# Optimization experiments

Hardware: AMD Instinct MI355X
Metric: run time of the kernel (lower is better)

## Reference

```python
import jax, jax.numpy as jnp
import numpy as np

# Dims: N batch, I input channels, C = in/hidden/attention/projection/out channels (all 128),
# streams=1, groups=1, spatial kernel 3, dropout 0.
N, I, C, H, W = 8, 128, 128, 36, 36


def _conv(x, w, pad):
    # x: [N, Cin, H, W], w: [Cout, Cin, kh, kw]
    return jax.lax.conv_general_dilated(
        x, w, (1, 1), pad, dimension_numbers=("NCHW", "OIHW", "NCHW"))


def _bias(b):
    return b[None, :, None, None]


def setup_inputs() -> dict:
    key = jax.random.key(0)
    ks = jax.random.split(key, 16)
    std = 0.05

    def w(k, o, i, s):
        return jax.random.normal(k, (o, i, s, s), jnp.float32) * std

    p = {}
    p["inp"] = jax.random.normal(ks[0], (N, I, H, W), jnp.float32)
    p["c0"] = jax.random.normal(ks[1], (1, C, 1, 1), jnp.float32)
    # proj_x: 1x1 conv input->in_channels, bias init 0
    p["w_x"] = w(ks[2], C, I, 1)
    p["b_x"] = jnp.zeros((C,), jnp.float32)
    # token convs (3x3, no bias); q uses SAME pad, k/v VALID
    p["w_qx"] = w(ks[3], C, C, 3)
    p["w_qc"] = w(ks[4], C, C, 3)
    scale = C ** (-0.5)  # gain = attn_channels^-0.5 on k projections
    p["w_kx"] = w(ks[5], C, C, 3) * scale
    p["w_kc"] = w(ks[6], C, C, 3) * scale
    p["w_vx"] = w(ks[7], C, C, 3)
    p["w_vc"] = w(ks[8], C, C, 3)
    # gating 1x1 convs: proj_z (bias=init_gate=1), proj_n (bias=0), in 2*proj channels
    p["w_z"] = w(ks[9], C, 2 * C, 1)
    p["b_z"] = jnp.ones((C,), jnp.float32)
    p["w_n"] = w(ks[10], C, 2 * C, 1)
    p["b_n"] = jnp.zeros((C,), jnp.float32)
    # proj_h: in_channels + 2*projection_channels -> hidden
    p["w_h"] = w(ks[11], C, 3 * C, 1)
    p["b_h"] = jnp.zeros((C,), jnp.float32)
    # output 1x1 conv hidden -> out_channels
    p["w_o"] = w(ks[12], C, C, 1)
    p["b_o"] = jnp.zeros((C,), jnp.float32)
    return p


def reference(inp, c0, w_x, b_x, w_qx, w_qc, w_kx, w_kc, w_vx, w_vc,
              w_z, b_z, w_n, b_n, w_h, b_h, w_o, b_o):
    # proj_x (1x1) -> x: [N, C, H, W]
    x = _conv(inp, w_x, "VALID") + _bias(b_x)
    n_, _, hh, ww = x.shape
    c = jnp.broadcast_to(c0, (n_, c0.shape[1], hh, ww))
    q_len = hh * ww
    # q: SAME pad -> Q = H*W tokens; k/v: VALID -> D = (H-2)*(W-2) tokens
    q = jnp.stack([_conv(x, w_qx, "SAME"), _conv(c, w_qc, "SAME")], 0)
    q = q.reshape(2, n_, -1, q_len)                      # [A, N, C, Q]
    k_x = _conv(x, w_kx, "VALID")
    d_len = k_x.shape[2] * k_x.shape[3]
    k = jnp.stack([k_x, _conv(c, w_kc, "VALID")], 0).reshape(2, n_, -1, d_len)   # [B, N, C, D]
    v = jnp.stack([_conv(x, w_vx, "VALID"), _conv(c, w_vc, "VALID")], 0)
    v = v.reshape(2, n_, -1, d_len)                      # [B, N, C, D]
    # all (A query source) x (B key/value source) attention pairs
    attn = jax.nn.softmax(jnp.einsum("ancq,bncd->anbqd", q, k), axis=-1)
    a = jnp.einsum("bncd,anbqd->anbcq", v, attn)         # [A, N, B, C, Q]
    a = a.reshape(2, n_, -1, hh, ww)                     # channels = B*C = 2*proj
    a_x, a_c = a[0], a[1]
    # GRU-style gated cell update (stored state; not part of the returned output)
    z = jax.nn.sigmoid(_conv(a_c, w_z, "VALID") + _bias(b_z))
    n_cand = jnp.tanh(_conv(a_c, w_n, "VALID") + _bias(b_n))
    c_new = z * c + (1.0 - z) * n_cand  # noqa: F841 (past['c'] in the original)
    # hidden: tanh(proj_h(cat[x, a_x])), dropout p=0 is identity
    xa = jnp.concatenate([x, a_x], axis=1)               # [N, 3*C, H, W]
    h = jnp.tanh(_conv(xa, w_h, "VALID") + _bias(b_h))
    return _conv(h, w_o, "VALID") + _bias(b_o)           # [N, C, H, W]
```

## Files before the change

### kernel.cpp

```cpp
#include <hip/hip_runtime.h>
#include <hip/hip_bf16.h>
#include <math.h>

#define NN 8
#define CH 128
#define HH 36
#define WWI 36
#define PP 1296
#define DD 1156
#define VP 1280
#define KC 1152
#define QT 81
#define DT 5

typedef __attribute__((ext_vector_type(8))) short short8;
typedef __attribute__((ext_vector_type(4))) float f32x4;

__device__ inline unsigned short f2bf(float f) {
    __hip_bfloat16 h = __float2bfloat16(f);
    return __builtin_bit_cast(unsigned short, h);
}
__device__ inline float fast_tanh(float x) {
    float e = __expf(2.f * x);
    return 1.f - 2.f / (e + 1.f);
}
#define MFMA(a, b, c) __builtin_amdgcn_mfma_f32_16x16x32_bf16((a), (b), (c), 0, 0, 0)

__global__ void k_setup(const float* __restrict__ wq, const float* __restrict__ wk,
                        const float* __restrict__ wv, const float* __restrict__ wh,
                        const float* __restrict__ wo, const float* __restrict__ wx,
                        const float* __restrict__ c0, const float* __restrict__ w_vc,
                        const float* __restrict__ b_h,
                        unsigned short* __restrict__ wcat, unsigned short* __restrict__ whb,
                        unsigned short* __restrict__ wob, unsigned short* __restrict__ wxb,
                        float* __restrict__ hconst)
{
    if (blockIdx.x == 576) {
        __shared__ float c0s[CH];
        __shared__ float part[256];
        __shared__ float vcs[CH];
        const int t = threadIdx.x;
        const int c = t & 127, half = t >> 7;
        if (t < CH) c0s[t] = c0[t];
        __syncthreads();
        {
            const float* row = w_vc + (size_t)c * 1152 + half * 576;
            float s = 0.f;
#pragma unroll 4
            for (int j4 = 0; j4 < 144; ++j4) {
                float4 v = ((const float4*)row)[j4];
                int j = half * 576 + j4 * 4;
                s += v.x * c0s[j / 9] + v.y * c0s[(j + 1) / 9]
                   + v.z * c0s[(j + 2) / 9] + v.w * c0s[(j + 3) / 9];
            }
            part[t] = s;
        }
        __syncthreads();
        if (t < CH) vcs[t] = part[t] + part[t + 128];
        __syncthreads();
        {
            const float* wrow = wh + (size_t)c * 384 + 256 + half * 64;
            float hs = 0.f;
#pragma unroll
            for (int j4 = 0; j4 < 16; ++j4) {
                float4 v = ((const float4*)wrow)[j4];
                int ci = half * 64 + j4 * 4;
                hs += v.x * vcs[ci] + v.y * vcs[ci + 1] + v.z * vcs[ci + 2] + v.w * vcs[ci + 3];
            }
            part[t] = hs;
        }
        __syncthreads();
        if (t < CH) hconst[t] = b_h[t] + part[t] + part[t + 128];
        return;
    }
    int t = blockIdx.x * 256 + threadIdx.x;
    int co = t / KC;
    int rem = t - co * KC;
    int tap = rem >> 7, ci = rem & 127;
    int iidx = co * KC + ci * 9 + tap;
    wcat[t] = f2bf(wq[iidx]);
    wcat[147456 + t] = f2bf(wk[iidx]);
    wcat[294912 + t] = f2bf(wv[iidx]);
    if (t < 32768) {
        int c2 = t >> 8, k2 = t & 255;
        whb[t] = f2bf(wh[c2 * 384 + k2]);
    }
    if (t < 16384) { wob[t] = f2bf(wo[t]); wxb[t] = f2bf(wx[t]); }
}

__global__ __launch_bounds__(64)
void k_proj(const float* __restrict__ inp, const unsigned short* __restrict__ wxb,
            const float* __restrict__ bx, unsigned short* __restrict__ xt)
{
    const int lane = threadIdx.x;
    const int quad = lane >> 4, lrow = lane & 15;
    const int p0 = blockIdx.x * 16;
    const int co0 = blockIdx.y * 64;
    const int n = blockIdx.z;
    const float* in_n = inp + (size_t)n * CH * PP;
    f32x4 acc[4] = {};

#pragma unroll
    for (int ks = 0; ks < 4; ++ks) {
        union { short8 v; unsigned short u[8]; } a;
        int ci0 = ks * 32 + quad * 8;
#pragma unroll
        for (int j = 0; j < 8; ++j)
            a.u[j] = f2bf(in_n[(size_t)(ci0 + j) * PP + p0 + lrow]);
#pragma unroll
        for (int ni = 0; ni < 4; ++ni) {
            short8 b = *(const short8*)&wxb[(size_t)(co0 + ni * 16 + lrow) * CH + ks * 32 + quad * 8];
            acc[ni] = MFMA(a.v, b, acc[ni]);
        }
    }
    unsigned short* xn = xt + (size_t)n * PP * CH;
#pragma unroll
    for (int ni = 0; ni < 4; ++ni) {
        float bv = bx[co0 + ni * 16 + lrow];
#pragma unroll
        for (int r = 0; r < 4; ++r)
            xn[(size_t)(p0 + quad * 4 + r) * CH + co0 + ni * 16 + lrow] = f2bf(acc[ni][r] + bv);
    }
}

__global__ __launch_bounds__(256)
void k_conv(const unsigned short* __restrict__ xt, const unsigned short* __restrict__ wcat,
            unsigned short* __restrict__ qt, unsigned short* __restrict__ kt,
            unsigned short* __restrict__ vb)
{
    __shared__ unsigned short lA[2][64 * 72];
    const int t = threadIdx.x;
    const int wave = t >> 6, lane = t & 63;
    const int quad = lane >> 4, lrow = lane & 15;
    const int mode = blockIdx.y;
    const int n = blockIdx.z;
    const int limit = (mode == 0) ? PP : DD;
    const int tile0 = blockIdx.x * 64;
    if (tile0 >= limit) return;
    const unsigned short* xn = xt + (size_t)n * PP * CH;
    const unsigned short* wb = wcat + (size_t)mode * 128 * KC;

    const int arow = t >> 2, aseg = t & 3;
    int apr, apc;
    {
        int tok = tile0 + arow; if (tok >= limit) tok = limit - 1;
        int dv = (mode == 0) ? 36 : 34;
        apr = tok / dv; apc = tok - apr * dv;
    }
    const unsigned short* wr0 = wb + (size_t)((wave * 2 + 0) * 16 + lrow) * KC;
    const unsigned short* wr1 = wb + (size_t)((wave * 2 + 1) * 16 + lrow) * KC;

    uint4 ra0, ra1;
    auto loadA = [&](int ks) {
        int tap = ks >> 1;
        int ky = tap / 3, kx = tap - ky * 3;
        int ci = (ks & 1) * 64 + aseg * 16;
        if (mode == 0) {
            int yy = apr + ky - 1, xx = apc + kx - 1;
            bool ok = (yy >= 0) && (yy < HH) && (xx >= 0) && (xx < WWI);
            ra0 = make_uint4(0, 0, 0, 0);
            ra1 = make_uint4(0, 0, 0, 0);
            if (ok) {
                const unsigned short* p = &xn[(size_t)(yy * WWI + xx) * CH + ci];
                ra0 = *(const uint4*)p;
                ra1 = *(const uint4*)(p + 8);
            }
        } else {
            int yy = apr + ky, xx = apc + kx;
            const unsigned short* p = &xn[(size_t)(yy * WWI + xx) * CH + ci];
            ra0 = *(const uint4*)p;
            ra1 = *(const uint4*)(p + 8);
        }
    };
    auto storeA = [&](int buf) {
        *(uint4*)&lA[buf][arow * 72 + aseg * 16] = ra0;
        *(uint4*)&lA[buf][arow * 72 + aseg * 16 + 8] = ra1;
    };

    short8 b0[2], b1[2], n0[2], n1[2];
    auto loadB = [&](int ks, short8* d0, short8* d1) {
        int off = (ks >> 1) * 128 + (ks & 1) * 64 + quad * 8;
        d0[0] = *(const short8*)(wr0 + off);
        d0[1] = *(const short8*)(wr0 + off + 32);
        d1[0] = *(const short8*)(wr1 + off);
        d1[1] = *(const short8*)(wr1 + off + 32);
    };

    f32x4 acc[4][2] = {};
    loadA(0);
    storeA(0);
    loadB(0, b0, b1);
    __syncthreads();

#pragma unroll
    for (int ks = 0; ks < 18; ++ks) {
        const int buf = ks & 1;
        if (ks < 17) {
            loadA(ks + 1);
            loadB(ks + 1, n0, n1);
        }
#pragma unroll
        for (int sub = 0; sub < 2; ++sub)
#pragma unroll
            for (int mi = 0; mi < 4; ++mi) {
                short8 a = *(const short8*)&lA[buf][(mi * 16 + lrow) * 72 + sub * 32 + quad * 8];
                acc[mi][0] = MFMA(a, b0[sub], acc[mi][0]);
                acc[mi][1] = MFMA(a, b1[sub], acc[mi][1]);
            }
        if (ks < 17) {
            storeA(buf ^ 1);
            b0[0] = n0[0]; b0[1] = n0[1];
            b1[0] = n1[0]; b1[1] = n1[1];
        }
        __syncthreads();
    }

    if (mode == 0) {
        unsigned short* qn = qt + (size_t)n * PP * CH;
#pragma unroll
        for (int mi = 0; mi < 4; ++mi)
#pragma unroll
            for (int r = 0; r < 4; ++r) {
                int p = tile0 + mi * 16 + quad * 4 + r;
                if (p < PP)
#pragma unroll
                    for (int ni = 0; ni < 2; ++ni)
                        qn[(size_t)p * CH + (wave * 2 + ni) * 16 + lrow] = f2bf(acc[mi][ni][r]);
            }
    } else if (mode == 1) {
        unsigned short* kn = kt + (size_t)n * DD * CH;
#pragma unroll
        for (int mi = 0; mi < 4; ++mi)
#pragma unroll
            for (int r = 0; r < 4; ++r) {
                int d = tile0 + mi * 16 + quad * 4 + r;
                if (d < DD)
#pragma unroll
                    for (int ni = 0; ni < 2; ++ni)
                        kn[(size_t)d * CH + (wave * 2 + ni) * 16 + lrow] = f2bf(acc[mi][ni][r]);
            }
    } else {
        unsigned short* vn = vb + (size_t)n * CH * VP;
#pragma unroll
        for (int mi = 0; mi < 4; ++mi)
#pragma unroll
            for (int r = 0; r < 4; ++r) {
                int d = tile0 + mi * 16 + quad * 4 + r;
                if (d < DD)
#pragma unroll
                    for (int ni = 0; ni < 2; ++ni)
                        vn[(size_t)((wave * 2 + ni) * 16 + lrow) * VP + d] = f2bf(acc[mi][ni][r]);
            }
    }
}

__global__ __launch_bounds__(256)
void k_attn(const unsigned short* __restrict__ qt, const unsigned short* __restrict__ kt,
            const unsigned short* __restrict__ vb, _Float16* __restrict__ po,
            float* __restrict__ pm, float* __restrict__ pl)
{
    __shared__ unsigned short lS[2][128 * 40];
    __shared__ unsigned short lp[4][16 * 136];
    const int t = threadIdx.x;
    const int wave = t >> 6, lane = t & 63;
    const int quad = lane >> 4, lrow = lane & 15;
    const int qg = blockIdx.x;
    const int dt = blockIdx.y;
    const int n = blockIdx.z;
    const int qti = qg * 4 + wave;
    const int d0 = dt * 256;
    const unsigned short* qn = qt + (size_t)n * PP * CH;
    const unsigned short* kn = kt + (size_t)n * DD * CH;
    const unsigned short* vn = vb + (size_t)n * CH * VP;

    const int arow = t >> 2, aseg8 = (t & 3) * 8;
    const int lo0 = arow * 40 + aseg8;
    const int lo1 = (arow + 64) * 40 + aseg8;

    short8 qa[4];
    {
        int qrow = qti * 16 + lrow; if (qrow >= PP) qrow = PP - 1;
#pragma unroll
        for (int ks = 0; ks < 4; ++ks)
            qa[ks] = *(const short8*)&qn[(size_t)qrow * CH + ks * 32 + quad * 8];
    }

    f32x4 o[8] = {};
    float mx[4] = {-1e30f, -1e30f, -1e30f, -1e30f};
    float rs[4] = {0.f, 0.f, 0.f, 0.f};

#pragma unroll
    for (int h = 0; h < 2; ++h) {
        const int dbase = d0 + h * 128;
        int kr0 = dbase + arow;      if (kr0 >= DD) kr0 = DD - 1;
        int kr1 = dbase + arow + 64; if (kr1 >= DD) kr1 = DD - 1;
        const unsigned short* kp0 = kn + (size_t)kr0 * CH + aseg8;
        const unsigned short* kp1 = kn + (size_t)kr1 * CH + aseg8;
        const unsigned short* vp0 = vn + (size_t)arow * VP + dbase + aseg8;
        const unsigned short* vp1 = vn + (size_t)(arow + 64) * VP + dbase + aseg8;

        f32x4 s[8] = {};
        uint4 r0 = *(const uint4*)kp0;
        uint4 r1 = *(const uint4*)kp1;
        *(uint4*)&lS[0][lo0] = r0;
        *(uint4*)&lS[0][lo1] = r1;
        __syncthreads();
#pragma unroll
        for (int ks = 0; ks < 4; ++ks) {
            const int buf = ks & 1;
            if (ks < 3) {
                r0 = *(const uint4*)(kp0 + (ks + 1) * 32);
                r1 = *(const uint4*)(kp1 + (ks + 1) * 32);
            }
#pragma unroll
            for (int ni = 0; ni < 8; ++ni) {
                short8 b = *(const short8*)&lS[buf][(ni * 16 + lrow) * 40 + quad * 8];
                s[ni] = MFMA(qa[ks], b, s[ni]);
            }
            if (ks < 3) {
                *(uint4*)&lS[buf ^ 1][lo0] = r0;
                *(uint4*)&lS[buf ^ 1][lo1] = r1;
            }
            __syncthreads();
        }

#pragma unroll
        for (int ni = 0; ni < 8; ++ni)
            if (dbase + ni * 16 + lrow >= DD)
#pragma unroll
                for (int r = 0; r < 4; ++r) s[ni][r] = -1e30f;

        float hm[4] = {-1e30f, -1e30f, -1e30f, -1e30f};
#pragma unroll
        for (int ni = 0; ni < 8; ++ni)
#pragma unroll
            for (int r = 0; r < 4; ++r) hm[r] = fmaxf(hm[r], s[ni][r]);
#pragma unroll
        for (int off = 1; off < 16; off <<= 1)
#pragma unroll
            for (int r = 0; r < 4; ++r) hm[r] = fmaxf(hm[r], __shfl_xor(hm[r], off, 64));

        float m[4], sc[4];
#pragma unroll
        for (int r = 0; r < 4; ++r) {
            m[r] = fmaxf(mx[r], hm[r]);
            sc[r] = __expf(mx[r] - m[r]);
        }

        float hs[4] = {0.f, 0.f, 0.f, 0.f};
#pragma unroll
        for (int ni = 0; ni < 8; ++ni)
#pragma unroll
            for (int r = 0; r < 4; ++r) {
                float e = __expf(s[ni][r] - m[r]);
                s[ni][r] = e;
                hs[r] += e;
            }
#pragma unroll
        for (int off = 1; off < 16; off <<= 1)
#pragma unroll
            for (int r = 0; r < 4; ++r) hs[r] += __shfl_xor(hs[r], off, 64);
#pragma unroll
        for (int r = 0; r < 4; ++r) {
            rs[r] = rs[r] * sc[r] + hs[r];
            mx[r] = m[r];
        }
#pragma unroll
        for (int ni = 0; ni < 8; ++ni)
#pragma unroll
            for (int r = 0; r < 4; ++r) o[ni][r] *= sc[r];

#pragma unroll
        for (int ni = 0; ni < 8; ++ni)
#pragma unroll
            for (int r = 0; r < 4; ++r)
                lp[wave][(quad * 4 + r) * 136 + ni * 16 + lrow] = f2bf(s[ni][r]);

        r0 = *(const uint4*)vp0;
        r1 = *(const uint4*)vp1;
        *(uint4*)&lS[0][lo0] = r0;
        *(uint4*)&lS[0][lo1] = r1;
        __syncthreads();
#pragma unroll
        for (int ks = 0; ks < 4; ++ks) {
            const int buf = ks & 1;
            if (ks < 3) {
                r0 = *(const uint4*)(vp0 + (ks + 1) * 32);
                r1 = *(const uint4*)(vp1 + (ks + 1) * 32);
            }
            short8 pa = *(const short8*)&lp[wave][lrow * 136 + ks * 32 + quad * 8];
#pragma unroll
            for (int ni = 0; ni < 8; ++ni) {
                short8 b = *(const short8*)&lS[buf][(ni * 16 + lrow) * 40 + quad * 8];
                o[ni] = MFMA(pa, b, o[ni]);
            }
            if (ks < 3) {
                *(uint4*)&lS[buf ^ 1][lo0] = r0;
                *(uint4*)&lS[buf ^ 1][lo1] = r1;
            }
            __syncthreads();
        }
    }

    if (qti < QT) {
        const int base = (n * QT + qti) * DT + dt;
        _Float16* pob = po + (size_t)base * 2048;
#pragma unroll
        for (int ni = 0; ni < 8; ++ni)
#pragma unroll
            for (int r = 0; r < 4; ++r)
                pob[(quad * 4 + r) * 128 + ni * 16 + lrow] = (_Float16)o[ni][r];
        if (lrow == 0)
#pragma unroll
            for (int r = 0; r < 4; ++r) {
                pm[base * 16 + quad * 4 + r] = mx[r];
                pl[base * 16 + quad * 4 + r] = rs[r];
            }
    }
}

__global__ __launch_bounds__(256)
void k_ahout(const _Float16* __restrict__ po, const float* __restrict__ pm,
             const float* __restrict__ pl, const unsigned short* __restrict__ xt,
             const unsigned short* __restrict__ whb, const float* __restrict__ hconst,
             const unsigned short* __restrict__ wob, const float* __restrict__ bo,
             float* __restrict__ out)
{
    __shared__ float sm[80], ssc[80], smg[16], sli[16];
    __shared__ unsigned short la0[16 * 136];
    __shared__ unsigned short lh[16 * 136];
    const int qti = blockIdx.x;
    const int n = blockIdx.y;
    const int base = (n * QT + qti) * DT;
    const int t = threadIdx.x;

    if (t < 80) sm[t] = pm[base * 16 + t];
    __syncthreads();
    if (t < 16) {
        float mg = -1e30f;
#pragma unroll
        for (int dt = 0; dt < DT; ++dt) mg = fmaxf(mg, sm[dt * 16 + t]);
        float ls = 0.f;
#pragma unroll
        for (int dt = 0; dt < DT; ++dt) ls += __expf(sm[dt * 16 + t] - mg) * pl[base * 16 + dt * 16 + t];
        smg[t] = mg; sli[t] = 1.f / ls;
    }
    __syncthreads();
    if (t < 80) ssc[t] = __expf(sm[t] - smg[t & 15]);
    __syncthreads();
#pragma unroll
    for (int k = 0; k < 8; ++k) {
        int idx = t + k * 256;
        int row = idx >> 7, c = idx & 127;
        float acc = 0.f;
#pragma unroll
        for (int dt = 0; dt < DT; ++dt)
            acc += ssc[dt * 16 + row] * (float)po[(size_t)(base + dt) * 2048 + idx];
        la0[row * 136 + c] = f2bf(acc * sli[row]);
    }
    __syncthreads();

    const int wave = t >> 6, lane = t & 63;
    const int quad = lane >> 4, lrow = lane & 15;
    const int p0 = qti * 16;
    const unsigned short* x0 = xt + (size_t)n * PP * CH;

    f32x4 acc1[2] = {};
#pragma unroll
    for (int ks = 0; ks < 8; ++ks) {
        int col = (ks & 3) * 32 + quad * 8;
        short8 a;
        if (ks < 4) a = *(const short8*)&x0[(size_t)(p0 + lrow) * CH + col];
        else        a = *(const short8*)&la0[lrow * 136 + col];
#pragma unroll
        for (int j = 0; j < 2; ++j) {
            int ni = wave * 2 + j;
            short8 b = *(const short8*)&whb[(size_t)(ni * 16 + lrow) * 256 + ks * 32 + quad * 8];
            acc1[j] = MFMA(a, b, acc1[j]);
        }
    }
#pragma unroll
    for (int j = 0; j < 2; ++j) {
        int ni = wave * 2 + j;
        float hc = hconst[ni * 16 + lrow];
#pragma unroll
        for (int r = 0; r < 4; ++r)
            lh[(quad * 4 + r) * 136 + ni * 16 + lrow] = f2bf(fast_tanh(acc1[j][r] + hc));
    }
    __syncthreads();

    f32x4 acc2[2] = {};
#pragma unroll
    for (int ks = 0; ks < 4; ++ks) {
        short8 a = *(const short8*)&lh[lrow * 136 + ks * 32 + quad * 8];
#pragma unroll
        for (int j = 0; j < 2; ++j) {
            int ni = wave * 2 + j;
            short8 b = *(const short8*)&wob[(size_t)(ni * 16 + lrow) * CH + ks * 32 + quad * 8];
            acc2[j] = MFMA(a, b, acc2[j]);
        }
    }
#pragma unroll
    for (int j = 0; j < 2; ++j) {
        int ni = wave * 2 + j;
        float bv = bo[ni * 16 + lrow];
#pragma unroll
        for (int r = 0; r < 4; ++r)
            out[((size_t)(n * CH + ni * 16 + lrow)) * PP + p0 + quad * 4 + r] = acc2[j][r] + bv;
    }
}

extern "C" void kernel_launch(void* const* d_in, const int* in_sizes, int n_in,
                              void* d_out, int out_size, void* d_ws, size_t ws_size,
                              hipStream_t stream)
{
    const float* inp  = (const float*)d_in[0];
    const float* c0   = (const float*)d_in[1];
    const float* w_x  = (const float*)d_in[2];
    const float* b_x  = (const float*)d_in[3];
    const float* w_qx = (const float*)d_in[4];
    const float* w_kx = (const float*)d_in[6];
    const float* w_vx = (const float*)d_in[8];
    const float* w_vc = (const float*)d_in[9];
    const float* w_h  = (const float*)d_in[14];
    const float* b_h  = (const float*)d_in[15];
    const float* w_o  = (const float*)d_in[16];
    const float* b_o  = (const float*)d_in[17];
    float* out = (float*)d_out;

    char* w = (char*)d_ws;
    unsigned short* xt   = (unsigned short*)(w);
    unsigned short* qt   = (unsigned short*)(w + 2654208);
    unsigned short* kt   = (unsigned short*)(w + 5308416);
    unsigned short* vb   = (unsigned short*)(w + 7675904);
    unsigned short* wcat = (unsigned short*)(w + 12951552);
    unsigned short* wxb  = (unsigned short*)(w + 13836288);
    unsigned short* whb  = (unsigned short*)(w + 13869056);
    unsigned short* wob  = (unsigned short*)(w + 13934592);
    float* hconst        = (float*)(w + 13967360);
    float* pm            = (float*)(w + 13967872);
    float* pl            = (float*)(w + 14382592);
    _Float16* po         = (_Float16*)(w + 14797312);

    hipLaunchKernelGGL(k_setup, dim3(577), dim3(256), 0, stream,
                       w_qx, w_kx, w_vx, w_h, w_o, w_x, c0, w_vc, b_h,
                       wcat, whb, wob, wxb, hconst);

    hipLaunchKernelGGL(k_proj, dim3(QT, 2, NN), dim3(64), 0, stream, inp, wxb, b_x, xt);

    hipLaunchKernelGGL(k_conv, dim3(21, 3, NN), dim3(256), 0, stream, xt, wcat, qt, kt, vb);

    hipLaunchKernelGGL(k_attn, dim3(21, DT, NN), dim3(256), 0, stream, qt, kt, vb, po, pm, pl);

    hipLaunchKernelGGL(k_ahout, dim3(QT, NN), dim3(256), 0, stream,
                       po, pm, pl, xt, whb, hconst, wob, b_o, out);
}
```

Measured before the change: 193.7 us.

## Load full K/V tiles into one LDS buffer and overlap V load with softmax

```diff
diff --git a/kernel.cpp b/kernel.cpp
--- a/kernel.cpp
+++ b/kernel.cpp
@@ -259,7 +259,7 @@
             const unsigned short* __restrict__ vb, _Float16* __restrict__ po,
             float* __restrict__ pm, float* __restrict__ pl)
 {
-    __shared__ unsigned short lS[2][128 * 40];
+    __shared__ unsigned short lbuf[128 * 136];
     __shared__ unsigned short lp[4][16 * 136];
     const int t = threadIdx.x;
     const int wave = t >> 6, lane = t & 63;
@@ -273,9 +273,9 @@
     const unsigned short* kn = kt + (size_t)n * DD * CH;
     const unsigned short* vn = vb + (size_t)n * CH * VP;
 
-    const int arow = t >> 2, aseg8 = (t & 3) * 8;
-    const int lo0 = arow * 40 + aseg8;
-    const int lo1 = (arow + 64) * 40 + aseg8;
+    const int srow = t >> 1;
+    const int scol = (t & 1) * 64;
+    const int sdst = srow * 136 + scol;
 
     short8 qa[4];
     {
@@ -292,36 +292,33 @@
 #pragma unroll
     for (int h = 0; h < 2; ++h) {
         const int dbase = d0 + h * 128;
-        int kr0 = dbase + arow;      if (kr0 >= DD) kr0 = DD - 1;
-        int kr1 = dbase + arow + 64; if (kr1 >= DD) kr1 = DD - 1;
-        const unsigned short* kp0 = kn + (size_t)kr0 * CH + aseg8;
-        const unsigned short* kp1 = kn + (size_t)kr1 * CH + aseg8;
-        const unsigned short* vp0 = vn + (size_t)arow * VP + dbase + aseg8;
-        const unsigned short* vp1 = vn + (size_t)(arow + 64) * VP + dbase + aseg8;
+
+        {
+            int krow = dbase + srow; if (krow >= DD) krow = DD - 1;
+            const unsigned short* src = kn + (size_t)krow * CH + scol;
+#pragma unroll
+            for (int j = 0; j < 8; ++j)
+                *(uint4*)&lbuf[sdst + j * 8] = *(const uint4*)(src + j * 8);
+        }
+        __syncthreads();
 
         f32x4 s[8] = {};
-        uint4 r0 = *(const uint4*)kp0;
-        uint4 r1 = *(const uint4*)kp1;
-        *(uint4*)&lS[0][lo0] = r0;
-        *(uint4*)&lS[0][lo1] = r1;
-        __syncthreads();
-#pragma unroll
-        for (int ks = 0; ks < 4; ++ks) {
-            const int buf = ks & 1;
-            if (ks < 3) {
-                r0 = *(const uint4*)(kp0 + (ks + 1) * 32);
-                r1 = *(const uint4*)(kp1 + (ks + 1) * 32);
-            }
+        __builtin_amdgcn_s_setprio(1);
+#pragma unroll
+        for (int ks = 0; ks < 4; ++ks)
 #pragma unroll
             for (int ni = 0; ni < 8; ++ni) {
-                short8 b = *(const short8*)&lS[buf][(ni * 16 + lrow) * 40 + quad * 8];
+                short8 b = *(const short8*)&lbuf[(ni * 16 + lrow) * 136 + ks * 32 + quad * 8];
                 s[ni] = MFMA(qa[ks], b, s[ni]);
             }
-            if (ks < 3) {
-                *(uint4*)&lS[buf ^ 1][lo0] = r0;
-                *(uint4*)&lS[buf ^ 1][lo1] = r1;
-            }
-            __syncthreads();
+        __builtin_amdgcn_s_setprio(0);
+        __syncthreads();
+
+        {
+            const unsigned short* src = vn + (size_t)srow * VP + dbase + scol;
+#pragma unroll
+            for (int j = 0; j < 8; ++j)
+                *(uint4*)&lbuf[sdst + j * 8] = *(const uint4*)(src + j * 8);
         }
 
 #pragma unroll
@@ -376,30 +373,20 @@
             for (int r = 0; r < 4; ++r)
                 lp[wave][(quad * 4 + r) * 136 + ni * 16 + lrow] = f2bf(s[ni][r]);
 
-        r0 = *(const uint4*)vp0;
-        r1 = *(const uint4*)vp1;
-        *(uint4*)&lS[0][lo0] = r0;
-        *(uint4*)&lS[0][lo1] = r1;
-        __syncthreads();
-#pragma unroll
-        for (int ks = 0; ks < 4; ++ks) {
-            const int buf = ks & 1;
-            if (ks < 3) {
-                r0 = *(const uint4*)(vp0 + (ks + 1) * 32);
-                r1 = *(const uint4*)(vp1 + (ks + 1) * 32);
-            }
-            short8 pa = *(const short8*)&lp[wave][lrow * 136 + ks * 32 + quad * 8];
+        __syncthreads();
+
+        __builtin_amdgcn_s_setprio(1);
+#pragma unroll
+        for (int kd = 0; kd < 4; ++kd) {
+            short8 pa = *(const short8*)&lp[wave][lrow * 136 + kd * 32 + quad * 8];
 #pragma unroll
             for (int ni = 0; ni < 8; ++ni) {
-                short8 b = *(const short8*)&lS[buf][(ni * 16 + lrow) * 40 + quad * 8];
+                short8 b = *(const short8*)&lbuf[(ni * 16 + lrow) * 136 + kd * 32 + quad * 8];
                 o[ni] = MFMA(pa, b, o[ni]);
             }
-            if (ks < 3) {
-                *(uint4*)&lS[buf ^ 1][lo0] = r0;
-                *(uint4*)&lS[buf ^ 1][lo1] = r1;
-            }
-            __syncthreads();
-        }
+        }
+        __builtin_amdgcn_s_setprio(0);
+        if (h == 0) __syncthreads();
     }
 
     if (qti < QT) {
```

Result: slower. 208.9 us (+7.9%).
